# Kernel optimization log

Hardware: AMD Instinct MI355X
Metric: run time of the kernel (lower is better)

Reference implementation:

```python
import jax, jax.numpy as jnp
import numpy as np
import math

IN_CH, OUT_CH, K, W_DIM = 256, 256, 3, 512
B, H = 16, 128

def setup_inputs() -> dict:
    key = jax.random.key(0)
    k1, k2, k3, k4 = jax.random.split(key, 4)
    return {
        "x": jax.random.normal(k1, (B, IN_CH, H, H), dtype=jnp.float32),
        "w": jax.random.normal(k2, (B, W_DIM), dtype=jnp.float32),
        "weight": jax.random.normal(k3, (1, OUT_CH, IN_CH, K, K), dtype=jnp.float32),
        "mod_weight": jax.random.normal(k4, (IN_CH, W_DIM), dtype=jnp.float32),
        "mod_bias": jnp.zeros((IN_CH,), dtype=jnp.float32),
    }

def reference(x, w, weight, mod_weight, mod_bias):
    batch, in_ch = x.shape[0], x.shape[1]
    k = weight.shape[-1]
    pad = k // 2
    conv_scale = 1.0 / math.sqrt(in_ch * k * k)
    mod_scale = 1.0 / math.sqrt(mod_weight.shape[1])  # EqualLinear scale, lr_mul=1

    # style: [B, in_ch]
    style = w @ (mod_weight * mod_scale).T + mod_bias
    # per-sample modulated weights: [B, out_ch, in_ch, k, k]
    wt = conv_scale * weight * style[:, None, :, None, None]
    # demodulation
    d = jax.lax.rsqrt(jnp.sum(wt * wt, axis=(2, 3, 4), keepdims=True) + 1e-8)
    wt = wt * d

    def conv_one(xi, wi):
        # xi: [in_ch, H, W], wi: [out_ch, in_ch, k, k]
        return jax.lax.conv_general_dilated(
            xi[None], wi, window_strides=(1, 1),
            padding=[(pad, pad), (pad, pad)],
            dimension_numbers=("NCHW", "OIHW", "NCHW"))[0]

    # [B, out_ch, H, W]
    return jax.vmap(conv_one)(x, wt)
```

## Files before the change

kernel.cpp:

```cpp
#include <hip/hip_runtime.h>
#include <math.h>

#define IN_CH  256
#define OUT_CH 256
#define WDIM   512
#define BATCH  16
#define HH     128

typedef _Float16 f16;
typedef f16   f16x8 __attribute__((ext_vector_type(8)));
typedef float f32x4 __attribute__((ext_vector_type(4)));

#define NCOL 130
#define XSLOTS (3 * NCOL * 4)

__device__ __host__ inline size_t wblock(int b, int dydx, int ocg, int chunk) {
    return ((((size_t)b * 9 + dydx) * 2 + ocg) * 8 + chunk) * 4096;
}

__global__ void style_kernel(const float* __restrict__ w,
                             const float* __restrict__ mod_weight,
                             const float* __restrict__ mod_bias,
                             float* __restrict__ style) {
    const int b = blockIdx.y;
    const int i = blockIdx.x * 64 + threadIdx.x;
    const float4* wp = (const float4*)(w + (size_t)b * WDIM);
    const float4* mp = (const float4*)(mod_weight + (size_t)i * WDIM);
    float acc = 0.f;
#pragma unroll 8
    for (int j = 0; j < WDIM / 4; ++j) {
        float4 a = wp[j], c = mp[j];
        acc += a.x * c.x + a.y * c.y + a.z * c.z + a.w * c.w;
    }
    style[b * IN_CH + i] = acc * (1.0f / sqrtf((float)WDIM)) + mod_bias[i];
}

__global__ void wsq_kernel(const float* __restrict__ weight,
                           float* __restrict__ q) {
    const int o = blockIdx.x, i = threadIdx.x;
    const float* wp = weight + ((size_t)o * IN_CH + i) * 9;
    float s = 0.f;
#pragma unroll
    for (int r = 0; r < 9; ++r) { float v = wp[r]; s += v * v; }
    q[o * IN_CH + i] = s;
}

__global__ void demod_kernel(const float* __restrict__ q,
                             const float* __restrict__ style,
                             float* __restrict__ dfac) {
    const int o = blockIdx.x, b = blockIdx.y, t = threadIdx.x;
    float4 qv = *(const float4*)(q + (size_t)o * IN_CH + 4 * t);
    float4 sv = *(const float4*)(style + (size_t)b * IN_CH + 4 * t);
    float s = qv.x * sv.x * sv.x + qv.y * sv.y * sv.y
            + qv.z * sv.z * sv.z + qv.w * sv.w * sv.w;
#pragma unroll
    for (int off = 32; off > 0; off >>= 1) s += __shfl_down(s, off, 64);
    if (t == 0) dfac[b * OUT_CH + o] = rsqrtf(s * (1.0f / 2304.0f) + 1e-8f);
}

__global__ void wmod_kernel(const float* __restrict__ weight,
                            const float* __restrict__ style,
                            const float* __restrict__ dfac,
                            f16* __restrict__ wmod) {
    const int r = blockIdx.x, ocg = blockIdx.y, b = blockIdx.z;
    const int t = threadIdx.x;
    const int ocl = t >> 1, half = t & 1;
    const int oc = ocg * 128 + ocl;
    const float sd = dfac[b * OUT_CH + oc] * (1.0f / 48.0f);
    const float* wp = weight + (size_t)oc * IN_CH * 9 + r;
    const float* sp = style + (size_t)b * IN_CH;
    for (int chunk = 0; chunk < 8; ++chunk) {
        const int icb = chunk * 32 + half * 16;
        union { f16 h[16]; uint4 u[2]; } buf;
#pragma unroll
        for (int j = 0; j < 16; ++j) {
            const int ic = icb + j;
            buf.h[j] = (f16)(wp[(size_t)ic * 9] * sp[ic] * sd);
        }
        uint4* dst = (uint4*)(wmod + wblock(b, r, ocg, chunk) + (size_t)ocl * 32 + half * 16);
        dst[0] = buf.u[0];
        dst[1] = buf.u[1];
    }
}

__global__ __launch_bounds__(256, 3) void conv_mfma(
        const float* __restrict__ x,
        const f16*  __restrict__ wmod,
        float* __restrict__ out) {
    __shared__ uint4 xs4[2 * XSLOTS];

    const int bid = blockIdx.x;
    const int lid = (bid & 7) * 512 + (bid >> 3);
    const int ocg = lid & 1;
    const int y0  = (lid >> 1) & 127;
    const int b   = lid >> 8;

    const int t  = threadIdx.x;
    const int l  = t & 63;
    const int w  = t >> 6;
    const int wm = w >> 1, wn = w & 1;
    const int lm = l & 15, lg = l >> 4;

    f32x4 acc[4][4];
#pragma unroll
    for (int i = 0; i < 4; ++i)
#pragma unroll
        for (int j = 0; j < 4; ++j) acc[i][j] = (f32x4){0.f, 0.f, 0.f, 0.f};

    if (t < 48) {
        int buf = t / 24, rem = t - 24 * buf;
        int blk = rem >> 2;
        int r = blk >> 1;
        int c = (blk & 1) ? 129 : 0;
        uint4 z = {0u, 0u, 0u, 0u};
        xs4[buf * XSLOTS + (r * NCOL + c) * 4 + (rem & 3)] = z;
    }

    const int cq = t & 31;
    const int gq = t >> 5;

    auto stageX = [&](int chunk, int buf) {
        const int ic0 = chunk * 32;
        uint4* xbuf = xs4 + buf * XSLOTS;
#pragma unroll
        for (int r = 0; r < 3; ++r) {
            const int gy = y0 - 1 + r;
            float vv[4][4];
            if (gy >= 0 && gy < HH) {
#pragma unroll
                for (int rr = 0; rr < 4; ++rr) {
                    const float* gp = x + (((size_t)(b * IN_CH + ic0 + 4 * gq + rr)) * HH + gy) * HH + 4 * cq;
                    float4 qv = *(const float4*)gp;
                    vv[rr][0] = qv.x; vv[rr][1] = qv.y; vv[rr][2] = qv.z; vv[rr][3] = qv.w;
                }
            } else {
#pragma unroll
                for (int rr = 0; rr < 4; ++rr)
#pragma unroll
                    for (int cc = 0; cc < 4; ++cc) vv[rr][cc] = 0.f;
            }
#pragma unroll
            for (int cc = 0; cc < 4; ++cc) {
                const int c = 1 + 4 * cq + cc;
                const int lsel = ((gq >> 1) + (c >> 2)) & 3;
                union { f16 h[4]; uint2 u2; } pk;
                pk.h[0] = (f16)vv[0][cc]; pk.h[1] = (f16)vv[1][cc];
                pk.h[2] = (f16)vv[2][cc]; pk.h[3] = (f16)vv[3][cc];
                char* p = (char*)xbuf + (((size_t)r * NCOL + c) << 6) + (lsel << 4) + ((gq & 1) << 3);
                *(uint2*)p = pk.u2;
            }
        }
    };

    auto aload = [&](int chunk, int dydx, f16x8* dst) {
        const f16* p = wmod + wblock(b, dydx, ocg, chunk);
#pragma unroll
        for (int mt = 0; mt < 4; ++mt) {
            const int ocl = wm * 64 + mt * 16 + lm;
            dst[mt] = *(const f16x8*)(p + (size_t)ocl * 32 + lg * 8);
        }
    };

    f16x8 afc[4], afn[4];
    aload(0, 0, afc);
    stageX(0, 0);
    __syncthreads();

    int cur = 0;
    for (int chunk = 0; chunk < 8; ++chunk) {
        if (chunk < 7) stageX(chunk + 1, cur ^ 1);
        const uint4* xbuf = xs4 + cur * XSLOTS;
#pragma unroll
        for (int dydx = 0; dydx < 9; ++dydx) {
            int nd = dydx + 1, nb = chunk;
            if (nd == 9) { nd = 0; nb = chunk + 1; }
            if (nb < 8) aload(nb, nd, afn);

            const int dy = dydx / 3;
            const int dx = dydx - 3 * dy;
#pragma unroll
            for (int nt = 0; nt < 4; ++nt) {
                const int c = wn * 64 + nt * 16 + lm + dx;
                const int lsel = (lg + (c >> 2)) & 3;
                const char* bp = (const char*)xbuf + (((size_t)dy * NCOL + c) << 6) + (lsel << 4);
                f16x8 bf = *(const f16x8*)bp;
#pragma unroll
                for (int mt = 0; mt < 4; ++mt) {
                    acc[mt][nt] = __builtin_amdgcn_mfma_f32_16x16x32_f16(afc[mt], bf, acc[mt][nt], 0, 0, 0);
                }
            }
#pragma unroll
            for (int mt = 0; mt < 4; ++mt) afc[mt] = afn[mt];
        }
        __syncthreads();
        cur ^= 1;
    }

#pragma unroll
    for (int mt = 0; mt < 4; ++mt) {
#pragma unroll
        for (int nt = 0; nt < 4; ++nt) {
            const int col = wn * 64 + nt * 16 + lm;
#pragma unroll
            for (int reg = 0; reg < 4; ++reg) {
                const int oc = ocg * 128 + wm * 64 + mt * 16 + lg * 4 + reg;
                out[(((size_t)(b * OUT_CH + oc)) * HH + y0) * HH + col] = acc[mt][nt][reg];
            }
        }
    }
}

#define TILE_H 32
#define TILE_W 64
#define OCB    8
#define ICH    4
#define XS_COLS 66
#define XS_STRIDE 68
#define XS_ROWS 34

__global__ void demod_fb_kernel(const float* __restrict__ weight,
                                const float* __restrict__ style,
                                float* __restrict__ dfac) {
    const int b = blockIdx.x;
    const int o = threadIdx.x;
    __shared__ float s2[IN_CH];
    for (int j = threadIdx.x; j < IN_CH; j += 256) {
        float s = style[b * IN_CH + j];
        s2[j] = s * s;
    }
    __syncthreads();
    float acc2 = 0.f;
    const float* wp = weight + (size_t)o * IN_CH * 9;
    for (int i = 0; i < IN_CH; ++i) {
        float sq = 0.f;
#pragma unroll
        for (int r = 0; r < 9; ++r) { float v = wp[i * 9 + r]; sq += v * v; }
        acc2 += sq * s2[i];
    }
    dfac[b * OUT_CH + o] = rsqrtf(acc2 * (1.0f / 2304.0f) + 1e-8f);
}

__global__ __launch_bounds__(256, 3) void conv_kernel(
        const float* __restrict__ x,
        const float* __restrict__ weight,
        const float* __restrict__ style,
        const float* __restrict__ dfac,
        float* __restrict__ out) {
    __shared__ float xs[ICH][XS_ROWS * XS_STRIDE];
    __shared__ float wsm[ICH][OCB][12];

    const int tile = blockIdx.x;
    const int ocg  = blockIdx.y;
    const int b    = blockIdx.z;
    const int y0 = (tile >> 1) * TILE_H;
    const int x0 = (tile & 1) * TILE_W;

    const int t  = threadIdx.x;
    const int ty = t >> 3;
    const int tx = t & 7;

    float acc[OCB][8];
#pragma unroll
    for (int o = 0; o < OCB; ++o)
#pragma unroll
        for (int j = 0; j < 8; ++j) acc[o][j] = 0.f;

    const float* xb = x + (size_t)b * IN_CH * HH * HH;
    const float* stb = style + b * IN_CH;
    const float* dfb = dfac + b * OUT_CH;

    for (int ic0 = 0; ic0 < IN_CH; ic0 += ICH) {
        __syncthreads();
        for (int icl = 0; icl < ICH; ++icl) {
            const float* xc = xb + (size_t)(ic0 + icl) * HH * HH;
            for (int s = t; s < XS_ROWS * XS_COLS; s += 256) {
                int row = s / XS_COLS;
                int col = s - row * XS_COLS;
                int gy = y0 + row - 1;
                int gx = x0 + col - 1;
                float v = 0.f;
                if (gy >= 0 && gy < HH && gx >= 0 && gx < HH) v = xc[gy * HH + gx];
                xs[icl][row * XS_STRIDE + col] = v;
            }
        }
        for (int s = t; s < ICH * OCB * 9; s += 256) {
            int icl = s / (OCB * 9);
            int rem = s - icl * (OCB * 9);
            int o   = rem / 9;
            int r   = rem - o * 9;
            int oc  = ocg * OCB + o;
            int ic  = ic0 + icl;
            float wv = weight[((size_t)oc * IN_CH + ic) * 9 + r];
            wsm[icl][o][r] = wv * ((1.0f / 48.0f) * stb[ic] * dfb[oc]);
        }
        __syncthreads();
#pragma unroll 1
        for (int icl = 0; icl < ICH; ++icl) {
            float xr[3][10];
#pragma unroll
            for (int dy = 0; dy < 3; ++dy) {
                const float* p = &xs[icl][(ty + dy) * XS_STRIDE + 8 * tx];
                float4 a  = *(const float4*)(p);
                float4 bv = *(const float4*)(p + 4);
                float2 c  = *(const float2*)(p + 8);
                xr[dy][0] = a.x;  xr[dy][1] = a.y;  xr[dy][2] = a.z;  xr[dy][3] = a.w;
                xr[dy][4] = bv.x; xr[dy][5] = bv.y; xr[dy][6] = bv.z; xr[dy][7] = bv.w;
                xr[dy][8] = c.x;  xr[dy][9] = c.y;
            }
#pragma unroll
            for (int o = 0; o < OCB; ++o) {
                const float* wp = wsm[icl][o];
                float w0 = wp[0], w1 = wp[1], w2 = wp[2];
                float w3 = wp[3], w4 = wp[4], w5 = wp[5];
                float w6 = wp[6], w7 = wp[7], w8 = wp[8];
#pragma unroll
                for (int j = 0; j < 8; ++j) {
                    acc[o][j] += w0 * xr[0][j]     + w1 * xr[0][j + 1] + w2 * xr[0][j + 2]
                               + w3 * xr[1][j]     + w4 * xr[1][j + 1] + w5 * xr[1][j + 2]
                               + w6 * xr[2][j]     + w7 * xr[2][j + 1] + w8 * xr[2][j + 2];
                }
            }
        }
    }

    const int gy = y0 + ty;
    const int gx = x0 + 8 * tx;
#pragma unroll
    for (int o = 0; o < OCB; ++o) {
        int oc = ocg * OCB + o;
        float* op = out + (((size_t)b * OUT_CH + oc) * HH + gy) * HH + gx;
        float4 v0 = {acc[o][0], acc[o][1], acc[o][2], acc[o][3]};
        float4 v1 = {acc[o][4], acc[o][5], acc[o][6], acc[o][7]};
        *(float4*)(op)     = v0;
        *(float4*)(op + 4) = v1;
    }
}

extern "C" void kernel_launch(void* const* d_in, const int* in_sizes, int n_in,
                              void* d_out, int out_size, void* d_ws, size_t ws_size,
                              hipStream_t stream) {
    const float* x          = (const float*)d_in[0];
    const float* w          = (const float*)d_in[1];
    const float* weight     = (const float*)d_in[2];
    const float* mod_weight = (const float*)d_in[3];
    const float* mod_bias   = (const float*)d_in[4];
    float* out = (float*)d_out;

    float* style = (float*)d_ws;
    float* dfac  = style + BATCH * IN_CH;
    float* q     = dfac + BATCH * OUT_CH;
    f16*   wmodp = (f16*)((char*)d_ws + 16384 + 16384 + 262144);

    const size_t need = 16384 + 16384 + 262144
                      + (size_t)BATCH * 9 * 2 * 8 * 4096 * sizeof(f16);

    style_kernel<<<dim3(4, BATCH), dim3(64), 0, stream>>>(w, mod_weight, mod_bias, style);

    if (ws_size >= need) {
        wsq_kernel<<<dim3(256), dim3(256), 0, stream>>>(weight, q);
        demod_kernel<<<dim3(256, BATCH), dim3(64), 0, stream>>>(q, style, dfac);
        wmod_kernel<<<dim3(9, 2, BATCH), dim3(256), 0, stream>>>(weight, style, dfac, wmodp);
        conv_mfma<<<dim3(4096), dim3(256), 0, stream>>>(x, wmodp, out);
    } else {
        demod_fb_kernel<<<dim3(BATCH), dim3(256), 0, stream>>>(weight, style, dfac);
        conv_kernel<<<dim3(8, 32, BATCH), dim3(256), 0, stream>>>(x, weight, style, dfac, out);
    }
}
```

Measured before the change: 778.4 us.

## Compute all output channels per row block and pre-transpose weights for modulation

The conv kernel now computes all 256 output channels for one output row per block, with each wave covering 128 columns. This halves the grid and halves the redundant x staging and f16 conversion per row, at the cost of doubled accumulator registers and lower occupancy (launch bounds 3 to 2). Weight fragment prefetch now uses three rotating register sets, loading two steps ahead. A new pre-pass transposes the base weights into the wmod block layout so the modulation kernel can read coalesced float4s and take style and demod factors from shared memory, using extra workspace.

```diff
diff --git a/kernel.cpp b/kernel.cpp
--- a/kernel.cpp
+++ b/kernel.cpp
@@ -16,6 +16,9 @@
 
 __device__ __host__ inline size_t wblock(int b, int dydx, int ocg, int chunk) {
     return ((((size_t)b * 9 + dydx) * 2 + ocg) * 8 + chunk) * 4096;
+}
+__device__ inline size_t wtoff(int r, int ocg, int chunk, int ocl, int icl) {
+    return ((((size_t)r * 2 + ocg) * 8 + chunk) * 128 + ocl) * 32 + icl;
 }
 
 __global__ void style_kernel(const float* __restrict__ w,
@@ -35,14 +38,32 @@
     style[b * IN_CH + i] = acc * (1.0f / sqrtf((float)WDIM)) + mod_bias[i];
 }
 
-__global__ void wsq_kernel(const float* __restrict__ weight,
-                           float* __restrict__ q) {
-    const int o = blockIdx.x, i = threadIdx.x;
-    const float* wp = weight + ((size_t)o * IN_CH + i) * 9;
-    float s = 0.f;
-#pragma unroll
-    for (int r = 0; r < 9; ++r) { float v = wp[r]; s += v * v; }
-    q[o * IN_CH + i] = s;
+__global__ void wt_kernel(const float* __restrict__ weight,
+                          float* __restrict__ wT,
+                          float* __restrict__ q) {
+    const int oc = blockIdx.x, t = threadIdx.x;
+    const int ocg = oc >> 7, ocl = oc & 127;
+    const float* wp = weight + (size_t)oc * IN_CH * 9 + (size_t)t * 36;
+    float v[36];
+#pragma unroll
+    for (int j = 0; j < 36; ++j) v[j] = wp[j];
+    float sq0 = 0.f, sq1 = 0.f, sq2 = 0.f, sq3 = 0.f;
+#pragma unroll
+    for (int u = 0; u < 4; ++u) {
+        const int ic = 4 * t + u;
+        const int chunk = ic >> 5, icl = ic & 31;
+        float s = 0.f;
+#pragma unroll
+        for (int r = 0; r < 9; ++r) {
+            float xv = v[u * 9 + r];
+            s += xv * xv;
+            wT[wtoff(r, ocg, chunk, ocl, icl)] = xv;
+        }
+        if (u == 0) sq0 = s; else if (u == 1) sq1 = s;
+        else if (u == 2) sq2 = s; else sq3 = s;
+    }
+    float4 qv = {sq0, sq1, sq2, sq3};
+    *(float4*)(q + (size_t)oc * IN_CH + 4 * t) = qv;
 }
 
 __global__ void demod_kernel(const float* __restrict__ q,
@@ -56,6 +77,48 @@
 #pragma unroll
     for (int off = 32; off > 0; off >>= 1) s += __shfl_down(s, off, 64);
     if (t == 0) dfac[b * OUT_CH + o] = rsqrtf(s * (1.0f / 2304.0f) + 1e-8f);
+}
+
+__global__ void wmod2_kernel(const float* __restrict__ wT,
+                             const float* __restrict__ style,
+                             const float* __restrict__ dfac,
+                             f16* __restrict__ wmod) {
+    const int r = blockIdx.x, ocg = blockIdx.y, b = blockIdx.z;
+    const int t = threadIdx.x;
+    __shared__ float ss[IN_CH];
+    __shared__ float dd[128];
+    if (t < 128) dd[t] = dfac[b * OUT_CH + ocg * 128 + t];
+    ss[t] = style[b * IN_CH + t] * (1.0f / 48.0f);
+    __syncthreads();
+    const int ocl = t >> 1, icb = (t & 1) * 16;
+    const float dv = dd[ocl];
+#pragma unroll 1
+    for (int chunk = 0; chunk < 8; ++chunk) {
+        const float* src = wT + wtoff(r, ocg, chunk, ocl, icb);
+        float4 a0 = *(const float4*)(src);
+        float4 a1 = *(const float4*)(src + 4);
+        float4 a2 = *(const float4*)(src + 8);
+        float4 a3 = *(const float4*)(src + 12);
+        float vals[16] = {a0.x,a0.y,a0.z,a0.w, a1.x,a1.y,a1.z,a1.w,
+                          a2.x,a2.y,a2.z,a2.w, a3.x,a3.y,a3.z,a3.w};
+        union { f16 h[16]; uint4 u[2]; } ob;
+#pragma unroll
+        for (int j = 0; j < 16; ++j)
+            ob.h[j] = (f16)(vals[j] * ss[chunk * 32 + icb + j] * dv);
+        uint4* dst = (uint4*)(wmod + wblock(b, r, ocg, chunk) + (size_t)ocl * 32 + icb);
+        dst[0] = ob.u[0];
+        dst[1] = ob.u[1];
+    }
+}
+
+__global__ void wsq_kernel(const float* __restrict__ weight,
+                           float* __restrict__ q) {
+    const int o = blockIdx.x, i = threadIdx.x;
+    const float* wp = weight + ((size_t)o * IN_CH + i) * 9;
+    float s = 0.f;
+#pragma unroll
+    for (int r = 0; r < 9; ++r) { float v = wp[r]; s += v * v; }
+    q[o * IN_CH + i] = s;
 }
 
 __global__ void wmod_kernel(const float* __restrict__ weight,
@@ -83,29 +146,29 @@
     }
 }
 
-__global__ __launch_bounds__(256, 3) void conv_mfma(
+__global__ __launch_bounds__(256, 2) void conv_mfma(
         const float* __restrict__ x,
         const f16*  __restrict__ wmod,
         float* __restrict__ out) {
     __shared__ uint4 xs4[2 * XSLOTS];
 
     const int bid = blockIdx.x;
-    const int lid = (bid & 7) * 512 + (bid >> 3);
-    const int ocg = lid & 1;
-    const int y0  = (lid >> 1) & 127;
-    const int b   = lid >> 8;
+    const int lid = (bid & 7) * 256 + (bid >> 3);
+    const int y0  = lid & 127;
+    const int b   = lid >> 7;
 
     const int t  = threadIdx.x;
     const int l  = t & 63;
     const int w  = t >> 6;
-    const int wm = w >> 1, wn = w & 1;
+    const int wocg = w >> 1;
+    const int wo64 = (w & 1) * 64;
     const int lm = l & 15, lg = l >> 4;
 
-    f32x4 acc[4][4];
+    f32x4 acc[4][8];
 #pragma unroll
     for (int i = 0; i < 4; ++i)
 #pragma unroll
-        for (int j = 0; j < 4; ++j) acc[i][j] = (f32x4){0.f, 0.f, 0.f, 0.f};
+        for (int j = 0; j < 8; ++j) acc[i][j] = (f32x4){0.f, 0.f, 0.f, 0.f};
 
     if (t < 48) {
         int buf = t / 24, rem = t - 24 * buf;
@@ -152,19 +215,34 @@
         }
     };
 
-    auto aload = [&](int chunk, int dydx, f16x8* dst) {
-        const f16* p = wmod + wblock(b, dydx, ocg, chunk);
+    auto aload = [&](int chunk, int dydx, f16x8 (&dst)[4]) {
+        const f16* p = wmod + wblock(b, dydx, wocg, chunk);
 #pragma unroll
         for (int mt = 0; mt < 4; ++mt) {
-            const int ocl = wm * 64 + mt * 16 + lm;
+            const int ocl = wo64 + mt * 16 + lm;
             dst[mt] = *(const f16x8*)(p + (size_t)ocl * 32 + lg * 8);
         }
     };
 
-    f16x8 afc[4], afn[4];
-    aload(0, 0, afc);
+    f16x8 af0[4], af1[4], af2[4];
+    aload(0, 0, af0);
+    aload(0, 1, af1);
     stageX(0, 0);
     __syncthreads();
+
+    auto mma_blk = [&](const uint4* xbuf, int dy, int dx, f16x8 (&a)[4]) {
+#pragma unroll
+        for (int nt = 0; nt < 8; ++nt) {
+            const int c = nt * 16 + lm + dx;
+            const int lsel = (lg + (c >> 2)) & 3;
+            const char* bp = (const char*)xbuf + (((size_t)dy * NCOL + c) << 6) + (lsel << 4);
+            f16x8 bf = *(const f16x8*)bp;
+#pragma unroll
+            for (int mt = 0; mt < 4; ++mt) {
+                acc[mt][nt] = __builtin_amdgcn_mfma_f32_16x16x32_f16(a[mt], bf, acc[mt][nt], 0, 0, 0);
+            }
+        }
+    };
 
     int cur = 0;
     for (int chunk = 0; chunk < 8; ++chunk) {
@@ -172,25 +250,20 @@
         const uint4* xbuf = xs4 + cur * XSLOTS;
 #pragma unroll
         for (int dydx = 0; dydx < 9; ++dydx) {
-            int nd = dydx + 1, nb = chunk;
-            if (nd == 9) { nd = 0; nb = chunk + 1; }
-            if (nb < 8) aload(nb, nd, afn);
-
+            int nd = dydx + 2, nb = chunk;
+            if (nd >= 9) { nd -= 9; nb += 1; }
+            const int psel = (dydx + 2) % 3;
+            if (nb < 8) {
+                if (psel == 0) aload(nb, nd, af0);
+                else if (psel == 1) aload(nb, nd, af1);
+                else aload(nb, nd, af2);
+            }
             const int dy = dydx / 3;
             const int dx = dydx - 3 * dy;
-#pragma unroll
-            for (int nt = 0; nt < 4; ++nt) {
-                const int c = wn * 64 + nt * 16 + lm + dx;
-                const int lsel = (lg + (c >> 2)) & 3;
-                const char* bp = (const char*)xbuf + (((size_t)dy * NCOL + c) << 6) + (lsel << 4);
-                f16x8 bf = *(const f16x8*)bp;
-#pragma unroll
-                for (int mt = 0; mt < 4; ++mt) {
-                    acc[mt][nt] = __builtin_amdgcn_mfma_f32_16x16x32_f16(afc[mt], bf, acc[mt][nt], 0, 0, 0);
-                }
-            }
-#pragma unroll
-            for (int mt = 0; mt < 4; ++mt) afc[mt] = afn[mt];
+            const int sel = dydx % 3;
+            if (sel == 0) mma_blk(xbuf, dy, dx, af0);
+            else if (sel == 1) mma_blk(xbuf, dy, dx, af1);
+            else mma_blk(xbuf, dy, dx, af2);
         }
         __syncthreads();
         cur ^= 1;
@@ -199,11 +272,11 @@
 #pragma unroll
     for (int mt = 0; mt < 4; ++mt) {
 #pragma unroll
-        for (int nt = 0; nt < 4; ++nt) {
-            const int col = wn * 64 + nt * 16 + lm;
+        for (int nt = 0; nt < 8; ++nt) {
+            const int col = nt * 16 + lm;
 #pragma unroll
             for (int reg = 0; reg < 4; ++reg) {
-                const int oc = ocg * 128 + wm * 64 + mt * 16 + lg * 4 + reg;
+                const int oc = wocg * 128 + wo64 + mt * 16 + lg * 4 + reg;
                 out[(((size_t)(b * OUT_CH + oc)) * HH + y0) * HH + col] = acc[mt][nt][reg];
             }
         }
@@ -349,18 +422,28 @@
     float* style = (float*)d_ws;
     float* dfac  = style + BATCH * IN_CH;
     float* q     = dfac + BATCH * OUT_CH;
-    f16*   wmodp = (f16*)((char*)d_ws + 16384 + 16384 + 262144);
-
-    const size_t need = 16384 + 16384 + 262144
-                      + (size_t)BATCH * 9 * 2 * 8 * 4096 * sizeof(f16);
+    const size_t base = 16384 + 16384 + 262144;
+    const size_t wT_bytes   = (size_t)9 * 2 * 8 * 128 * 32 * sizeof(float);
+    const size_t wmod_bytes = (size_t)BATCH * 9 * 2 * 8 * 4096 * sizeof(f16);
+
+    const size_t need_new = base + wT_bytes + wmod_bytes;
+    const size_t need_old = base + wmod_bytes;
 
     style_kernel<<<dim3(4, BATCH), dim3(64), 0, stream>>>(w, mod_weight, mod_bias, style);
 
-    if (ws_size >= need) {
+    if (ws_size >= need_new) {
+        float* wT   = (float*)((char*)d_ws + base);
+        f16*  wmodp = (f16*)((char*)d_ws + base + wT_bytes);
+        wt_kernel<<<dim3(256), dim3(64), 0, stream>>>(weight, wT, q);
+        demod_kernel<<<dim3(256, BATCH), dim3(64), 0, stream>>>(q, style, dfac);
+        wmod2_kernel<<<dim3(9, 2, BATCH), dim3(256), 0, stream>>>(wT, style, dfac, wmodp);
+        conv_mfma<<<dim3(2048), dim3(256), 0, stream>>>(x, wmodp, out);
+    } else if (ws_size >= need_old) {
+        f16* wmodp = (f16*)((char*)d_ws + base);
         wsq_kernel<<<dim3(256), dim3(256), 0, stream>>>(weight, q);
         demod_kernel<<<dim3(256, BATCH), dim3(64), 0, stream>>>(q, style, dfac);
         wmod_kernel<<<dim3(9, 2, BATCH), dim3(256), 0, stream>>>(weight, style, dfac, wmodp);
-        conv_mfma<<<dim3(4096), dim3(256), 0, stream>>>(x, wmodp, out);
+        conv_mfma<<<dim3(2048), dim3(256), 0, stream>>>(x, wmodp, out);
     } else {
         demod_fb_kernel<<<dim3(BATCH), dim3(256), 0, stream>>>(weight, style, dfac);
         conv_kernel<<<dim3(8, 32, BATCH), dim3(256), 0, stream>>>(x, weight, style, dfac, out);
```

After: 908.3 us. 1.17x slower.
